# Kernel tuning notes

Measured on AMD Instinct MI355X. Metric: run time of the kernel, lower is better.

Reference implementation:

```python
import jax, jax.numpy as jnp
import numpy as np

N_NODES = 100000
N_EDGES = 1600000
IN_DIM, HID_DIM, OUT_DIM = 128, 128, 64


def setup_inputs() -> dict:
    key = jax.random.key(0)
    k1, k2, k3, k4, k5 = jax.random.split(key, 5)
    x = jax.random.normal(k1, (N_NODES, IN_DIM), dtype=jnp.float32)
    edge_index = jax.random.randint(k2, (2, N_EDGES), 0, N_NODES, dtype=jnp.int64)
    # PyG GCNConv linear weights (no bias); Glorot-ish scale for stability
    W1 = jax.random.normal(k3, (IN_DIM, HID_DIM), dtype=jnp.float32) * 0.05
    W2 = jax.random.normal(k4, (HID_DIM, HID_DIM), dtype=jnp.float32) * 0.05
    W3 = jax.random.normal(k5, (HID_DIM, OUT_DIM), dtype=jnp.float32) * 0.05
    return {"x": x, "edge_index": edge_index, "W1": W1, "W2": W2, "W3": W3}


def _gcn_conv(h, W, src, dst, num_nodes):
    # GCNConv(add_self_loops=False, normalize=False, bias=False):
    # linear transform, then scatter-add messages from src into dst
    msg = jnp.take(h @ W, src, axis=0)          # [E, d_out] gather
    return jax.ops.segment_sum(msg, dst, num_segments=num_nodes)  # [N, d_out]


def reference(x, edge_index, W1, W2, W3):
    num_nodes = x.shape[0]
    src, dst = edge_index[0], edge_index[1]
    h = jax.nn.relu(_gcn_conv(x, W1, src, dst, num_nodes))
    # dropout p=0.0 / eval mode -> identity
    h = jax.nn.relu(_gcn_conv(h, W2, src, dst, num_nodes))
    out = _gcn_conv(h, W3, src, dst, num_nodes)
    return jax.nn.log_softmax(out, axis=1)
```

## Files before the change

### kernel.cpp

```cpp
#include <hip/hip_runtime.h>
#include <hip/hip_bf16.h>

#define KDIM 128

typedef __attribute__((ext_vector_type(8))) __bf16 bf16x8;
typedef __attribute__((ext_vector_type(4))) float f32x4;
typedef __attribute__((ext_vector_type(2))) float f32x2;

static __device__ __forceinline__ unsigned short f2bf(float f) {
  unsigned u = __float_as_uint(f);
  u += 0x7fffu + ((u >> 16) & 1u);
  return (unsigned short)(u >> 16);
}
static __device__ __forceinline__ unsigned pack_bf16x2(float a, float b) {
  return (unsigned)f2bf(a) | ((unsigned)f2bf(b) << 16);
}
static __device__ __forceinline__ float2 unpack_bf16x2(unsigned u) {
  return make_float2(__uint_as_float(u << 16), __uint_as_float(u & 0xffff0000u));
}
static __device__ __forceinline__ unsigned relu2(unsigned u) {
  unsigned r = u;
  if (u & 0x00008000u) r &= 0xffff0000u;
  if (u & 0x80000000u) r &= 0x0000ffffu;
  return r;
}

static __device__ __forceinline__ unsigned char f2fp8(float f) {
#if __has_builtin(__builtin_amdgcn_cvt_pk_fp8_f32)
  return (unsigned char)(__builtin_amdgcn_cvt_pk_fp8_f32(f, f, 0, false) & 0xff);
#else
  unsigned s = (__float_as_uint(f) >> 24) & 0x80u;
  float a = fminf(fabsf(f), 448.f);
  if (a < 0.015625f) {
    unsigned m = (unsigned)(a * 512.f + 0.5f);
    return (unsigned char)(s | m);
  }
  unsigned v = __float_as_uint(a);
  v += 0x7ffffu + ((v >> 20) & 1u);
  unsigned em = (v >> 20) - 960u;
  if (em > 0x7eu) em = 0x7eu;
  return (unsigned char)(s | em);
#endif
}
static __device__ __forceinline__ float fp8dec(unsigned b) {
  unsigned s = (b & 0x80u) << 24;
  unsigned em = b & 0x7fu;
  float mag = (em >= 8) ? __uint_as_float((em + 960u) << 20)
                        : (float)em * 0.001953125f;
  return __uint_as_float(__float_as_uint(mag) | s);
}
static __device__ __forceinline__ float4 fp8x4_to_f32(unsigned u) {
#if __has_builtin(__builtin_amdgcn_cvt_pk_f32_fp8)
  f32x2 lo = __builtin_amdgcn_cvt_pk_f32_fp8(u, false);
  f32x2 hi = __builtin_amdgcn_cvt_pk_f32_fp8(u, true);
  return make_float4(lo[0], lo[1], hi[0], hi[1]);
#else
  return make_float4(fp8dec(u & 255u), fp8dec((u >> 8) & 255u),
                     fp8dec((u >> 16) & 255u), fp8dec(u >> 24));
#endif
}

__global__ __launch_bounds__(256) void wtrans_k(const float* __restrict__ W,
                                                unsigned short* __restrict__ Wt,
                                                int NOUT) {
  const int t = blockIdx.x * 256 + threadIdx.x;
  if (t >= NOUT * KDIM) return;
  const int n = t >> 7;
  const int k = t & 127;
  Wt[t] = f2bf(W[k * NOUT + n]);
}

template<int NOUT, bool AF32, bool RELU>
__global__ __launch_bounds__(512) void gemm_mfma_k(const void* __restrict__ Av,
                                                   const unsigned short* __restrict__ Wt,
                                                   unsigned char* __restrict__ C, int M) {
  constexpr int NT = NOUT / 16;
  __shared__ unsigned short Ws[NOUT][136];

  const int tid = threadIdx.x;
  for (int i = tid; i < NOUT * 16; i += 512) {
    const int n = i >> 4, k8 = i & 15;
    const uint4 v = *reinterpret_cast<const uint4*>(&Wt[n * KDIM + k8 * 8]);
    *reinterpret_cast<uint4*>(&Ws[n][k8 * 8]) = v;
  }

  const int wv = tid >> 6;
  const int l  = tid & 63;
  const int am = l & 15;
  const int kb = l >> 4;
  const int arow_g = blockIdx.x * 128 + wv * 16 + am;
  const bool valid = arow_g < M;
  const int arow = valid ? arow_g : 0;

  uint4 afr[4];
  if constexpr (AF32) {
    const float* A = (const float*)Av;
    #pragma unroll
    for (int ks = 0; ks < 4; ++ks) {
      const float4 lo = *reinterpret_cast<const float4*>(&A[(size_t)arow * 128 + ks * 32 + kb * 8]);
      const float4 hi = *reinterpret_cast<const float4*>(&A[(size_t)arow * 128 + ks * 32 + kb * 8 + 4]);
      afr[ks] = make_uint4(pack_bf16x2(lo.x, lo.y), pack_bf16x2(lo.z, lo.w),
                           pack_bf16x2(hi.x, hi.y), pack_bf16x2(hi.z, hi.w));
    }
  } else {
    const unsigned* A = (const unsigned*)Av;
    #pragma unroll
    for (int ks = 0; ks < 4; ++ks) {
      uint4 u = *reinterpret_cast<const uint4*>(&A[(size_t)arow * 64 + ks * 16 + kb * 4]);
      if constexpr (RELU) {
        u.x = relu2(u.x); u.y = relu2(u.y); u.z = relu2(u.z); u.w = relu2(u.w);
      }
      afr[ks] = u;
    }
  }
  if (!valid) {
    afr[0] = make_uint4(0, 0, 0, 0); afr[1] = afr[0];
    afr[2] = afr[0];                 afr[3] = afr[0];
  }

  f32x4 acc[NT];
  #pragma unroll
  for (int nt = 0; nt < NT; ++nt) {
    acc[nt][0] = 0.f; acc[nt][1] = 0.f; acc[nt][2] = 0.f; acc[nt][3] = 0.f;
  }

  __syncthreads();
  #pragma unroll
  for (int ks = 0; ks < 4; ++ks) {
    const bf16x8 a = __builtin_bit_cast(bf16x8, afr[ks]);
    #pragma unroll
    for (int nt = 0; nt < NT; ++nt) {
      const uint4 bv = *reinterpret_cast<const uint4*>(&Ws[nt * 16 + am][ks * 32 + kb * 8]);
      acc[nt] = __builtin_amdgcn_mfma_f32_16x16x32_bf16(
          a, __builtin_bit_cast(bf16x8, bv), acc[nt], 0, 0, 0);
    }
  }

  const int crow0 = blockIdx.x * 128 + wv * 16 + kb * 4;
  #pragma unroll
  for (int nt = 0; nt < NT; ++nt) {
    #pragma unroll
    for (int r = 0; r < 4; ++r) {
      const int rr = crow0 + r;
      if (rr < M) C[(size_t)rr * NOUT + nt * 16 + am] = f2fp8(acc[nt][r]);
    }
  }
}

__global__ __launch_bounds__(512) void hist_k(const int* __restrict__ dst,
                                              int* __restrict__ histT, int E) {
  __shared__ int h[256];
  if (threadIdx.x < 256) h[threadIdx.x] = 0;
  __syncthreads();
  const int E4 = E >> 2;
  for (int i = blockIdx.x * 512 + threadIdx.x; i < E4; i += 256 * 512) {
    const int4 d4 = *reinterpret_cast<const int4*>(&dst[i * 4]);
    atomicAdd(&h[d4.x >> 9], 1);
    atomicAdd(&h[d4.y >> 9], 1);
    atomicAdd(&h[d4.z >> 9], 1);
    atomicAdd(&h[d4.w >> 9], 1);
  }
  if (blockIdx.x == 0 && threadIdx.x < (E & 3))
    atomicAdd(&h[dst[E4 * 4 + threadIdx.x] >> 9], 1);
  __syncthreads();
  if (threadIdx.x < 256) histT[threadIdx.x * 256 + blockIdx.x] = h[threadIdx.x];
}

__global__ __launch_bounds__(256) void scan1_k(const int* __restrict__ in,
                                               int* __restrict__ out,
                                               int* __restrict__ bsum, int N) {
  __shared__ int ls[256];
  const int t = threadIdx.x;
  const int base = blockIdx.x * 2048 + t * 8;
  int v[8];
  if (base + 8 <= N) {
    *reinterpret_cast<int4*>(&v[0]) = *reinterpret_cast<const int4*>(&in[base]);
    *reinterpret_cast<int4*>(&v[4]) = *reinterpret_cast<const int4*>(&in[base + 4]);
  } else {
    #pragma unroll
    for (int j = 0; j < 8; ++j) v[j] = (base + j < N) ? in[base + j] : 0;
  }
  int s = 0;
  #pragma unroll
  for (int j = 0; j < 8; ++j) { const int tmp = v[j]; v[j] = s; s += tmp; }
  int x = s;
  ls[t] = x;
  __syncthreads();
  for (int off = 1; off < 256; off <<= 1) {
    int y = 0;
    if (t >= off) y = ls[t - off];
    __syncthreads();
    x += y;
    ls[t] = x;
    __syncthreads();
  }
  const int excl = x - s;
  #pragma unroll
  for (int j = 0; j < 8; ++j)
    if (base + j < N) out[base + j] = excl + v[j];
  if (t == 255) bsum[blockIdx.x] = x;
}

__global__ __launch_bounds__(64) void scan2_k(const int* __restrict__ bsum,
                                              int* __restrict__ bscan, int NB) {
  const int t = threadIdx.x;
  const int v = (t < NB) ? bsum[t] : 0;
  int x = v;
  #pragma unroll
  for (int off = 1; off < 64; off <<= 1) {
    const int y = __shfl_up(x, off, 64);
    if (t >= off) x += y;
  }
  bscan[t] = x - v;
}

__global__ __launch_bounds__(256) void addoff_k(int* __restrict__ off,
                                                const int* __restrict__ bscan) {
  const int i = blockIdx.x * 256 + threadIdx.x;
  off[i] += bscan[i >> 11];
}

__global__ __launch_bounds__(512) void binscatter_k(const int* __restrict__ src,
                                                    const int* __restrict__ dst,
                                                    const int* __restrict__ histOff,
                                                    unsigned* __restrict__ epack,
                                                    int E) {
  __shared__ int cur[256];
  if (threadIdx.x < 256) cur[threadIdx.x] = histOff[threadIdx.x * 256 + blockIdx.x];
  __syncthreads();
  const int E4 = E >> 2;
  for (int i = blockIdx.x * 512 + threadIdx.x; i < E4; i += 256 * 512) {
    const int4 d4 = *reinterpret_cast<const int4*>(&dst[i * 4]);
    const int4 s4 = *reinterpret_cast<const int4*>(&src[i * 4]);
    int p;
    p = atomicAdd(&cur[d4.x >> 9], 1); epack[p] = ((unsigned)(d4.x & 511) << 17) | (unsigned)s4.x;
    p = atomicAdd(&cur[d4.y >> 9], 1); epack[p] = ((unsigned)(d4.y & 511) << 17) | (unsigned)s4.y;
    p = atomicAdd(&cur[d4.z >> 9], 1); epack[p] = ((unsigned)(d4.z & 511) << 17) | (unsigned)s4.z;
    p = atomicAdd(&cur[d4.w >> 9], 1); epack[p] = ((unsigned)(d4.w & 511) << 17) | (unsigned)s4.w;
  }
  if (blockIdx.x == 0 && threadIdx.x < (E & 3)) {
    const int e = E4 * 4 + threadIdx.x;
    const int d = dst[e];
    const int p = atomicAdd(&cur[d >> 9], 1);
    epack[p] = ((unsigned)(d & 511) << 17) | (unsigned)src[e];
  }
}

__global__ __launch_bounds__(512) void binsort_k(const unsigned* __restrict__ epack,
                                                 const int* __restrict__ histOff,
                                                 int* __restrict__ rowptr,
                                                 int* __restrict__ col,
                                                 int N, int E) {
  __shared__ int hist[512];
  __shared__ int ls[256];
  __shared__ int cur[512];
  const int b = blockIdx.x;
  const int t = threadIdx.x;
  const int nbins = (N + 511) >> 9;
  const int beg = histOff[b * 256];
  const int end = (b + 1 < nbins) ? histOff[(b + 1) * 256] : E;

  hist[t] = 0;
  __syncthreads();
  for (int j = beg + t; j < end; j += 512)
    atomicAdd(&hist[epack[j] >> 17], 1);
  __syncthreads();

  int a = 0, b2 = 0, x = 0;
  if (t < 256) { a = hist[2 * t]; b2 = hist[2 * t + 1]; x = a + b2; ls[t] = x; }
  __syncthreads();
  for (int off = 1; off < 256; off <<= 1) {
    int y = 0;
    if (t < 256 && t >= off) y = ls[t - off];
    __syncthreads();
    if (t < 256) { x += y; ls[t] = x; }
    __syncthreads();
  }
  if (t < 256) {
    const int excl = x - a - b2;
    cur[2 * t] = excl;
    cur[2 * t + 1] = excl + a;
    const int g0 = b * 512 + 2 * t;
    if (g0 <= N) rowptr[g0] = beg + excl;
    if (g0 + 1 <= N) rowptr[g0 + 1] = beg + excl + a;
  }
  __syncthreads();
  for (int j = beg + t; j < end; j += 512) {
    const unsigned p = epack[j];
    const int pos = atomicAdd(&cur[p >> 17], 1);
    col[beg + pos] = (int)(p & 0x1ffffu);
  }
}

__global__ __launch_bounds__(256) void gather128_k(const uint2* __restrict__ H64,
                                                   const int* __restrict__ rowptr,
                                                   const int* __restrict__ col,
                                                   unsigned* __restrict__ out, int N) {
  const int w = (int)((blockIdx.x * 256u + threadIdx.x) >> 6);
  const int lane = threadIdx.x & 63;
  const int q = lane >> 4;
  const int l4 = lane & 15;
  if (w >= N) return;
  const int beg = __builtin_amdgcn_readfirstlane(rowptr[w]);
  const int end = __builtin_amdgcn_readfirstlane(rowptr[w + 1]);

  float4 a0A = make_float4(0.f, 0.f, 0.f, 0.f), a0B = make_float4(0.f, 0.f, 0.f, 0.f);
  float4 a1A = make_float4(0.f, 0.f, 0.f, 0.f), a1B = make_float4(0.f, 0.f, 0.f, 0.f);

  int e = beg;
  for (; e + 16 <= end; e += 16) {
    const int s0 = col[e + q];
    const int s1 = col[e + 4 + q];
    const int s2 = col[e + 8 + q];
    const int s3 = col[e + 12 + q];
    const uint2 u0 = H64[(size_t)s0 * 16 + l4];
    const uint2 u1 = H64[(size_t)s1 * 16 + l4];
    const uint2 u2 = H64[(size_t)s2 * 16 + l4];
    const uint2 u3 = H64[(size_t)s3 * 16 + l4];
    float4 v;
    v = fp8x4_to_f32(u0.x); a0A.x += v.x; a0A.y += v.y; a0A.z += v.z; a0A.w += v.w;
    v = fp8x4_to_f32(u0.y); a0B.x += v.x; a0B.y += v.y; a0B.z += v.z; a0B.w += v.w;
    v = fp8x4_to_f32(u1.x); a1A.x += v.x; a1A.y += v.y; a1A.z += v.z; a1A.w += v.w;
    v = fp8x4_to_f32(u1.y); a1B.x += v.x; a1B.y += v.y; a1B.z += v.z; a1B.w += v.w;
    v = fp8x4_to_f32(u2.x); a0A.x += v.x; a0A.y += v.y; a0A.z += v.z; a0A.w += v.w;
    v = fp8x4_to_f32(u2.y); a0B.x += v.x; a0B.y += v.y; a0B.z += v.z; a0B.w += v.w;
    v = fp8x4_to_f32(u3.x); a1A.x += v.x; a1A.y += v.y; a1A.z += v.z; a1A.w += v.w;
    v = fp8x4_to_f32(u3.y); a1B.x += v.x; a1B.y += v.y; a1B.z += v.z; a1B.w += v.w;
  }
  for (; e + 4 <= end; e += 4) {
    const uint2 u = H64[(size_t)col[e + q] * 16 + l4];
    float4 v;
    v = fp8x4_to_f32(u.x); a0A.x += v.x; a0A.y += v.y; a0A.z += v.z; a0A.w += v.w;
    v = fp8x4_to_f32(u.y); a0B.x += v.x; a0B.y += v.y; a0B.z += v.z; a0B.w += v.w;
  }
  if (q < end - e) {
    const uint2 u = H64[(size_t)col[e + q] * 16 + l4];
    float4 v;
    v = fp8x4_to_f32(u.x); a1A.x += v.x; a1A.y += v.y; a1A.z += v.z; a1A.w += v.w;
    v = fp8x4_to_f32(u.y); a1B.x += v.x; a1B.y += v.y; a1B.z += v.z; a1B.w += v.w;
  }

  float4 aA, aB;
  aA.x = a0A.x + a1A.x; aA.y = a0A.y + a1A.y;
  aA.z = a0A.z + a1A.z; aA.w = a0A.w + a1A.w;
  aB.x = a0B.x + a1B.x; aB.y = a0B.y + a1B.y;
  aB.z = a0B.z + a1B.z; aB.w = a0B.w + a1B.w;

  aA.x += __shfl_xor(aA.x, 16, 64); aA.x += __shfl_xor(aA.x, 32, 64);
  aA.y += __shfl_xor(aA.y, 16, 64); aA.y += __shfl_xor(aA.y, 32, 64);
  aA.z += __shfl_xor(aA.z, 16, 64); aA.z += __shfl_xor(aA.z, 32, 64);
  aA.w += __shfl_xor(aA.w, 16, 64); aA.w += __shfl_xor(aA.w, 32, 64);
  aB.x += __shfl_xor(aB.x, 16, 64); aB.x += __shfl_xor(aB.x, 32, 64);
  aB.y += __shfl_xor(aB.y, 16, 64); aB.y += __shfl_xor(aB.y, 32, 64);
  aB.z += __shfl_xor(aB.z, 16, 64); aB.z += __shfl_xor(aB.z, 32, 64);
  aB.w += __shfl_xor(aB.w, 16, 64); aB.w += __shfl_xor(aB.w, 32, 64);

  if (q == 0) {
    const uint4 pk = make_uint4(pack_bf16x2(aA.x, aA.y), pack_bf16x2(aA.z, aA.w),
                                pack_bf16x2(aB.x, aB.y), pack_bf16x2(aB.z, aB.w));
    *reinterpret_cast<uint4*>(&out[(size_t)w * 64 + l4 * 4]) = pk;
  }
}

__global__ __launch_bounds__(256) void gather64lsm_k(const unsigned* __restrict__ H32,
                                                     const int* __restrict__ rowptr,
                                                     const int* __restrict__ col,
                                                     float* __restrict__ out, int N) {
  const int w = (int)((blockIdx.x * 256u + threadIdx.x) >> 6);
  const int lane = threadIdx.x & 63;
  const int q = lane >> 4;
  const int l4 = lane & 15;
  if (w >= N) return;
  const int beg = __builtin_amdgcn_readfirstlane(rowptr[w]);
  const int end = __builtin_amdgcn_readfirstlane(rowptr[w + 1]);

  float4 acc0 = make_float4(0.f, 0.f, 0.f, 0.f);
  float4 acc1 = make_float4(0.f, 0.f, 0.f, 0.f);

  int e = beg;
  for (; e + 16 <= end; e += 16) {
    const int s0 = col[e + q];
    const int s1 = col[e + 4 + q];
    const int s2 = col[e + 8 + q];
    const int s3 = col[e + 12 + q];
    const unsigned u0 = H32[(size_t)s0 * 16 + l4];
    const unsigned u1 = H32[(size_t)s1 * 16 + l4];
    const unsigned u2 = H32[(size_t)s2 * 16 + l4];
    const unsigned u3 = H32[(size_t)s3 * 16 + l4];
    float4 v;
    v = fp8x4_to_f32(u0); acc0.x += v.x; acc0.y += v.y; acc0.z += v.z; acc0.w += v.w;
    v = fp8x4_to_f32(u1); acc1.x += v.x; acc1.y += v.y; acc1.z += v.z; acc1.w += v.w;
    v = fp8x4_to_f32(u2); acc0.x += v.x; acc0.y += v.y; acc0.z += v.z; acc0.w += v.w;
    v = fp8x4_to_f32(u3); acc1.x += v.x; acc1.y += v.y; acc1.z += v.z; acc1.w += v.w;
  }
  for (; e + 8 <= end; e += 8) {
    const int s0 = col[e + q];
    const int s1 = col[e + 4 + q];
    const float4 v0 = fp8x4_to_f32(H32[(size_t)s0 * 16 + l4]);
    const float4 v1 = fp8x4_to_f32(H32[(size_t)s1 * 16 + l4]);
    acc0.x += v0.x; acc0.y += v0.y; acc0.z += v0.z; acc0.w += v0.w;
    acc1.x += v1.x; acc1.y += v1.y; acc1.z += v1.z; acc1.w += v1.w;
  }
  if (e + 4 <= end) {
    const float4 v = fp8x4_to_f32(H32[(size_t)col[e + q] * 16 + l4]);
    acc0.x += v.x; acc0.y += v.y; acc0.z += v.z; acc0.w += v.w;
    e += 4;
  }
  if (e + q < end) {
    const float4 v = fp8x4_to_f32(H32[(size_t)col[e + q] * 16 + l4]);
    acc1.x += v.x; acc1.y += v.y; acc1.z += v.z; acc1.w += v.w;
  }

  float4 a;
  a.x = acc0.x + acc1.x;
  a.y = acc0.y + acc1.y;
  a.z = acc0.z + acc1.z;
  a.w = acc0.w + acc1.w;
  a.x += __shfl_xor(a.x, 16, 64); a.x += __shfl_xor(a.x, 32, 64);
  a.y += __shfl_xor(a.y, 16, 64); a.y += __shfl_xor(a.y, 32, 64);
  a.z += __shfl_xor(a.z, 16, 64); a.z += __shfl_xor(a.z, 32, 64);
  a.w += __shfl_xor(a.w, 16, 64); a.w += __shfl_xor(a.w, 32, 64);

  float m = fmaxf(fmaxf(a.x, a.y), fmaxf(a.z, a.w));
  #pragma unroll
  for (int o = 8; o > 0; o >>= 1) m = fmaxf(m, __shfl_xor(m, o, 64));
  float s = __expf(a.x - m) + __expf(a.y - m) + __expf(a.z - m) + __expf(a.w - m);
  #pragma unroll
  for (int o = 8; o > 0; o >>= 1) s += __shfl_xor(s, o, 64);
  const float ls = __logf(s);

  if (lane < 16) {
    *reinterpret_cast<float4*>(&out[(size_t)w * 64 + l4 * 4]) =
        make_float4(a.x - m - ls, a.y - m - ls, a.z - m - ls, a.w - m - ls);
  }
}

extern "C" void kernel_launch(void* const* d_in, const int* in_sizes, int n_in,
                              void* d_out, int out_size, void* d_ws, size_t ws_size,
                              hipStream_t stream) {
  const float* x  = (const float*)d_in[0];
  const int*   ei = (const int*)d_in[1];
  const float* W1 = (const float*)d_in[2];
  const float* W2 = (const float*)d_in[3];
  const float* W3 = (const float*)d_in[4];
  float* out = (float*)d_out;

  const int N = in_sizes[0] / KDIM;
  const int E = in_sizes[1] / 2;
  const int* src = ei;
  const int* dst = ei + E;

  unsigned char* H = (unsigned char*)d_ws;
  unsigned* AGGp = (unsigned*)(H + (size_t)N * 128);
  unsigned short* Wt1 = (unsigned short*)(AGGp + (size_t)N * 64);
  unsigned short* Wt2 = Wt1 + 128 * 128;
  unsigned short* Wt3 = Wt2 + 128 * 128;
  int* col     = (int*)(Wt3 + 64 * 128);
  int* rowptr  = col + E;
  int* histT   = rowptr + (N + 8);
  int* histOff = histT + 65536;
  int* bsum2   = histOff + 65536;
  int* bscan2  = bsum2 + 64;
  unsigned* epack = (unsigned*)AGGp;

  const int nbins = (N + 511) / 512;

  wtrans_k<<<(128 * 128 + 255) / 256, 256, 0, stream>>>(W1, Wt1, 128);
  wtrans_k<<<(128 * 128 + 255) / 256, 256, 0, stream>>>(W2, Wt2, 128);
  wtrans_k<<<(64 * 128 + 255) / 256, 256, 0, stream>>>(W3, Wt3, 64);

  hist_k<<<256, 512, 0, stream>>>(dst, histT, E);
  scan1_k<<<32, 256, 0, stream>>>(histT, histOff, bsum2, 65536);
  scan2_k<<<1, 64, 0, stream>>>(bsum2, bscan2, 32);
  addoff_k<<<256, 256, 0, stream>>>(histOff, bscan2);
  binscatter_k<<<256, 512, 0, stream>>>(src, dst, histOff, epack, E);
  binsort_k<<<nbins, 512, 0, stream>>>(epack, histOff, rowptr, col, N, E);

  const int gemm_grid = (N + 127) / 128;
  const int gather_grid = (N + 3) / 4;

  gemm_mfma_k<128, true, false><<<gemm_grid, 512, 0, stream>>>(x, Wt1, H, N);
  gather128_k<<<gather_grid, 256, 0, stream>>>((const uint2*)H, rowptr, col, AGGp, N);

  gemm_mfma_k<128, false, true><<<gemm_grid, 512, 0, stream>>>(AGGp, Wt2, H, N);
  gather128_k<<<gather_grid, 256, 0, stream>>>((const uint2*)H, rowptr, col, AGGp, N);

  gemm_mfma_k<64, false, true><<<gemm_grid, 512, 0, stream>>>(AGGp, Wt3, H, N);
  gather64lsm_k<<<gather_grid, 256, 0, stream>>>((const unsigned*)H, rowptr, col, out, N);
}
```

Before: 223.8 us.

## Merge weight transposes, fold scan offset add, use 256-node CSR bins

Merges the three weight-transpose launches into one kernel, removes the addoff kernel by adding the block-scan offsets inside binscatter and binsort, and halves the CSR bin width to 256 nodes, which doubles the bin count to about 391. Fewer launches cut fixed launch overhead, and smaller bins give the sort kernel more blocks with less work each. The cost is larger histogram and scan arrays, more global histogram cells to write and scan, and scan2 now relies on the block count staying at or below 64.

```diff
diff --git a/kernel.cpp b/kernel.cpp
--- a/kernel.cpp
+++ b/kernel.cpp
@@ -14,9 +14,6 @@
 }
 static __device__ __forceinline__ unsigned pack_bf16x2(float a, float b) {
   return (unsigned)f2bf(a) | ((unsigned)f2bf(b) << 16);
-}
-static __device__ __forceinline__ float2 unpack_bf16x2(unsigned u) {
-  return make_float2(__uint_as_float(u << 16), __uint_as_float(u & 0xffff0000u));
 }
 static __device__ __forceinline__ unsigned relu2(unsigned u) {
   unsigned r = u;
@@ -60,14 +57,21 @@
 #endif
 }
 
-__global__ __launch_bounds__(256) void wtrans_k(const float* __restrict__ W,
-                                                unsigned short* __restrict__ Wt,
-                                                int NOUT) {
+__global__ __launch_bounds__(256) void wtrans_k(const float* __restrict__ W1,
+                                                const float* __restrict__ W2,
+                                                const float* __restrict__ W3,
+                                                unsigned short* __restrict__ Wt) {
   const int t = blockIdx.x * 256 + threadIdx.x;
-  if (t >= NOUT * KDIM) return;
-  const int n = t >> 7;
-  const int k = t & 127;
-  Wt[t] = f2bf(W[k * NOUT + n]);
+  if (t >= 40960) return;
+  if (t < 16384) {
+    Wt[t] = f2bf(W1[(t & 127) * 128 + (t >> 7)]);
+  } else if (t < 32768) {
+    const int u = t - 16384;
+    Wt[t] = f2bf(W2[(u & 127) * 128 + (u >> 7)]);
+  } else {
+    const int u = t - 32768;
+    Wt[t] = f2bf(W3[(u & 127) * 64 + (u >> 7)]);
+  }
 }
 
 template<int NOUT, bool AF32, bool RELU>
@@ -148,22 +152,24 @@
 }
 
 __global__ __launch_bounds__(512) void hist_k(const int* __restrict__ dst,
-                                              int* __restrict__ histT, int E) {
-  __shared__ int h[256];
-  if (threadIdx.x < 256) h[threadIdx.x] = 0;
+                                              int* __restrict__ histT,
+                                              int E, int nbins) {
+  __shared__ int h[512];
+  for (int i = threadIdx.x; i < nbins; i += 512) h[i] = 0;
   __syncthreads();
   const int E4 = E >> 2;
   for (int i = blockIdx.x * 512 + threadIdx.x; i < E4; i += 256 * 512) {
     const int4 d4 = *reinterpret_cast<const int4*>(&dst[i * 4]);
-    atomicAdd(&h[d4.x >> 9], 1);
-    atomicAdd(&h[d4.y >> 9], 1);
-    atomicAdd(&h[d4.z >> 9], 1);
-    atomicAdd(&h[d4.w >> 9], 1);
+    atomicAdd(&h[d4.x >> 8], 1);
+    atomicAdd(&h[d4.y >> 8], 1);
+    atomicAdd(&h[d4.z >> 8], 1);
+    atomicAdd(&h[d4.w >> 8], 1);
   }
   if (blockIdx.x == 0 && threadIdx.x < (E & 3))
-    atomicAdd(&h[dst[E4 * 4 + threadIdx.x] >> 9], 1);
-  __syncthreads();
-  if (threadIdx.x < 256) histT[threadIdx.x * 256 + blockIdx.x] = h[threadIdx.x];
+    atomicAdd(&h[dst[E4 * 4 + threadIdx.x] >> 8], 1);
+  __syncthreads();
+  for (int i = threadIdx.x; i < nbins; i += 512)
+    histT[i * 256 + blockIdx.x] = h[i];
 }
 
 __global__ __launch_bounds__(256) void scan1_k(const int* __restrict__ in,
@@ -214,60 +220,63 @@
   bscan[t] = x - v;
 }
 
-__global__ __launch_bounds__(256) void addoff_k(int* __restrict__ off,
-                                                const int* __restrict__ bscan) {
-  const int i = blockIdx.x * 256 + threadIdx.x;
-  off[i] += bscan[i >> 11];
-}
-
 __global__ __launch_bounds__(512) void binscatter_k(const int* __restrict__ src,
                                                     const int* __restrict__ dst,
                                                     const int* __restrict__ histOff,
+                                                    const int* __restrict__ bscan,
                                                     unsigned* __restrict__ epack,
-                                                    int E) {
-  __shared__ int cur[256];
-  if (threadIdx.x < 256) cur[threadIdx.x] = histOff[threadIdx.x * 256 + blockIdx.x];
+                                                    int E, int nbins) {
+  __shared__ int cur[512];
+  for (int i = threadIdx.x; i < nbins; i += 512) {
+    const int gi = i * 256 + blockIdx.x;
+    cur[i] = histOff[gi] + bscan[gi >> 11];
+  }
   __syncthreads();
   const int E4 = E >> 2;
   for (int i = blockIdx.x * 512 + threadIdx.x; i < E4; i += 256 * 512) {
     const int4 d4 = *reinterpret_cast<const int4*>(&dst[i * 4]);
     const int4 s4 = *reinterpret_cast<const int4*>(&src[i * 4]);
     int p;
-    p = atomicAdd(&cur[d4.x >> 9], 1); epack[p] = ((unsigned)(d4.x & 511) << 17) | (unsigned)s4.x;
-    p = atomicAdd(&cur[d4.y >> 9], 1); epack[p] = ((unsigned)(d4.y & 511) << 17) | (unsigned)s4.y;
-    p = atomicAdd(&cur[d4.z >> 9], 1); epack[p] = ((unsigned)(d4.z & 511) << 17) | (unsigned)s4.z;
-    p = atomicAdd(&cur[d4.w >> 9], 1); epack[p] = ((unsigned)(d4.w & 511) << 17) | (unsigned)s4.w;
+    p = atomicAdd(&cur[d4.x >> 8], 1); epack[p] = ((unsigned)(d4.x & 255) << 17) | (unsigned)s4.x;
+    p = atomicAdd(&cur[d4.y >> 8], 1); epack[p] = ((unsigned)(d4.y & 255) << 17) | (unsigned)s4.y;
+    p = atomicAdd(&cur[d4.z >> 8], 1); epack[p] = ((unsigned)(d4.z & 255) << 17) | (unsigned)s4.z;
+    p = atomicAdd(&cur[d4.w >> 8], 1); epack[p] = ((unsigned)(d4.w & 255) << 17) | (unsigned)s4.w;
   }
   if (blockIdx.x == 0 && threadIdx.x < (E & 3)) {
     const int e = E4 * 4 + threadIdx.x;
     const int d = dst[e];
-    const int p = atomicAdd(&cur[d >> 9], 1);
-    epack[p] = ((unsigned)(d & 511) << 17) | (unsigned)src[e];
+    const int p = atomicAdd(&cur[d >> 8], 1);
+    epack[p] = ((unsigned)(d & 255) << 17) | (unsigned)src[e];
   }
 }
 
 __global__ __launch_bounds__(512) void binsort_k(const unsigned* __restrict__ epack,
                                                  const int* __restrict__ histOff,
+                                                 const int* __restrict__ bscan,
                                                  int* __restrict__ rowptr,
                                                  int* __restrict__ col,
-                                                 int N, int E) {
-  __shared__ int hist[512];
+                                                 int N, int E, int nbins) {
+  __shared__ int hist[256];
   __shared__ int ls[256];
-  __shared__ int cur[512];
+  __shared__ int cur[256];
   const int b = blockIdx.x;
   const int t = threadIdx.x;
-  const int nbins = (N + 511) >> 9;
-  const int beg = histOff[b * 256];
-  const int end = (b + 1 < nbins) ? histOff[(b + 1) * 256] : E;
-
-  hist[t] = 0;
+  const int i0 = b * 256;
+  const int beg = histOff[i0] + bscan[i0 >> 11];
+  int end = E;
+  if (b + 1 < nbins) {
+    const int i1 = (b + 1) * 256;
+    end = histOff[i1] + bscan[i1 >> 11];
+  }
+
+  if (t < 256) hist[t] = 0;
   __syncthreads();
   for (int j = beg + t; j < end; j += 512)
     atomicAdd(&hist[epack[j] >> 17], 1);
   __syncthreads();
 
-  int a = 0, b2 = 0, x = 0;
-  if (t < 256) { a = hist[2 * t]; b2 = hist[2 * t + 1]; x = a + b2; ls[t] = x; }
+  int v = 0, x = 0;
+  if (t < 256) { v = hist[t]; x = v; ls[t] = x; }
   __syncthreads();
   for (int off = 1; off < 256; off <<= 1) {
     int y = 0;
@@ -277,13 +286,12 @@
     __syncthreads();
   }
   if (t < 256) {
-    const int excl = x - a - b2;
-    cur[2 * t] = excl;
-    cur[2 * t + 1] = excl + a;
-    const int g0 = b * 512 + 2 * t;
-    if (g0 <= N) rowptr[g0] = beg + excl;
-    if (g0 + 1 <= N) rowptr[g0 + 1] = beg + excl + a;
-  }
+    const int excl = x - v;
+    cur[t] = excl;
+    const int g = b * 256 + t;
+    if (g <= N) rowptr[g] = beg + excl;
+  }
+  if (b == nbins - 1 && t == 0) rowptr[N] = E;
   __syncthreads();
   for (int j = beg + t; j < end; j += 512) {
     const unsigned p = epack[j];
@@ -450,6 +458,10 @@
   const int* src = ei;
   const int* dst = ei + E;
 
+  const int nbins = (N + 255) / 256;
+  const int ncells = nbins * 256;
+  const int scan_blocks = (ncells + 2047) / 2048;
+
   unsigned char* H = (unsigned char*)d_ws;
   unsigned* AGGp = (unsigned*)(H + (size_t)N * 128);
   unsigned short* Wt1 = (unsigned short*)(AGGp + (size_t)N * 64);
@@ -458,23 +470,18 @@
   int* col     = (int*)(Wt3 + 64 * 128);
   int* rowptr  = col + E;
   int* histT   = rowptr + (N + 8);
-  int* histOff = histT + 65536;
-  int* bsum2   = histOff + 65536;
+  int* histOff = histT + 131072;
+  int* bsum2   = histOff + 131072;
   int* bscan2  = bsum2 + 64;
   unsigned* epack = (unsigned*)AGGp;
 
-  const int nbins = (N + 511) / 512;
-
-  wtrans_k<<<(128 * 128 + 255) / 256, 256, 0, stream>>>(W1, Wt1, 128);
-  wtrans_k<<<(128 * 128 + 255) / 256, 256, 0, stream>>>(W2, Wt2, 128);
-  wtrans_k<<<(64 * 128 + 255) / 256, 256, 0, stream>>>(W3, Wt3, 64);
-
-  hist_k<<<256, 512, 0, stream>>>(dst, histT, E);
-  scan1_k<<<32, 256, 0, stream>>>(histT, histOff, bsum2, 65536);
-  scan2_k<<<1, 64, 0, stream>>>(bsum2, bscan2, 32);
-  addoff_k<<<256, 256, 0, stream>>>(histOff, bscan2);
-  binscatter_k<<<256, 512, 0, stream>>>(src, dst, histOff, epack, E);
-  binsort_k<<<nbins, 512, 0, stream>>>(epack, histOff, rowptr, col, N, E);
+  wtrans_k<<<(40960 + 255) / 256, 256, 0, stream>>>(W1, W2, W3, Wt1);
+
+  hist_k<<<256, 512, 0, stream>>>(dst, histT, E, nbins);
+  scan1_k<<<scan_blocks, 256, 0, stream>>>(histT, histOff, bsum2, ncells);
+  scan2_k<<<1, 64, 0, stream>>>(bsum2, bscan2, scan_blocks);
+  binscatter_k<<<256, 512, 0, stream>>>(src, dst, histOff, bscan2, epack, E, nbins);
+  binsort_k<<<nbins, 512, 0, stream>>>(epack, histOff, bscan2, rowptr, col, N, E, nbins);
 
   const int gemm_grid = (N + 127) / 128;
   const int gather_grid = (N + 3) / 4;
```

Result: faster. 216.1 us (-3.4%).
